# Performance work log

Measured on AMD Instinct MI355X. Metric: run time of the kernel, lower is better.

## Reference

```python
import jax, jax.numpy as jnp
import numpy as np

N = 100000
NFEAT = 512
NHID = 256
NCLASS = 40
E = 1600000
K = 10          # nlayers propagation hops
ALPHA = 0.1


def setup_inputs() -> dict:
    key = jax.random.key(0)
    ks = jax.random.split(key, 8)
    x = jax.random.normal(ks[0], (N, NFEAT), dtype=jnp.float32)
    edge_src = jax.random.randint(ks[1], (E,), 0, N, dtype=jnp.int32)
    edge_dst = jax.random.randint(ks[2], (E,), 0, N, dtype=jnp.int32)
    # roughly row-stochastic-scale edge values (avg degree ~16)
    edge_val = jax.random.uniform(ks[3], (E,), dtype=jnp.float32) * (1.0 / 16.0)
    stdv1 = 1.0 / np.sqrt(NFEAT)
    W1 = jax.random.uniform(ks[4], (NFEAT, NHID), minval=-stdv1, maxval=stdv1, dtype=jnp.float32)
    b1 = jax.random.uniform(ks[5], (NHID,), minval=-stdv1, maxval=stdv1, dtype=jnp.float32)
    stdv2 = 1.0 / np.sqrt(NHID)
    W2 = jax.random.uniform(ks[6], (NHID, NCLASS), minval=-stdv2, maxval=stdv2, dtype=jnp.float32)
    b2 = jax.random.uniform(ks[7], (NCLASS,), minval=-stdv2, maxval=stdv2, dtype=jnp.float32)
    return {"x": x, "edge_src": edge_src, "edge_dst": edge_dst, "edge_val": edge_val,
            "W1": W1, "b1": b1, "W2": W2, "b2": b2}


def _spmm(edge_src, edge_dst, edge_val, z):
    # sparse adj @ z via gather + segment-sum scatter: out[dst] += val * z[src]
    msgs = edge_val[:, None] * z[edge_src]          # [E, C]
    return jax.ops.segment_sum(msgs, edge_dst, num_segments=N)


def reference(x, edge_src, edge_dst, edge_val, W1, b1, W2, b2):
    # MLP transform (dropout is identity in eval mode)
    h = jax.nn.relu(x @ W1 + b1)                    # [N, NHID]
    h = h @ W2 + b2                                 # [N, NCLASS]
    # APPNP propagation: z <- (1-alpha) * A z + alpha * h
    def step(z, _):
        z = _spmm(edge_src, edge_dst, edge_val, z) * (1.0 - ALPHA) + ALPHA * h
        return z, None
    z, _ = jax.lax.scan(step, h, None, length=K)
    return jax.nn.log_softmax(z, axis=1)
```

## Files before the change

kernel.cpp:

```cpp
#include <hip/hip_runtime.h>
#include <hip/hip_bf16.h>
#include <math.h>

#define NN     100000
#define NFEATD 512
#define NHIDD  256
#define NCLS   40
#define NE     1600000
#define KHOP   10

typedef __attribute__((ext_vector_type(8))) short short8;
typedef __attribute__((ext_vector_type(4))) float floatx4;

static __device__ __forceinline__ float bf2f(unsigned int u) {
  unsigned int x = u << 16;
  float f;
  __builtin_memcpy(&f, &x, 4);
  return f;
}
static __device__ __forceinline__ unsigned short f2bf(float f) {
  unsigned int x;
  __builtin_memcpy(&x, &f, 4);
  x = (x + 0x7fffu + ((x >> 16) & 1u)) >> 16;
  return (unsigned short)x;
}
static __device__ __forceinline__ void bf8_to_f(const uint4 u, float* f) {
  unsigned int a0 = u.x, a1 = u.y, a2 = u.z, a3 = u.w;
  unsigned int t;
  t = a0 << 16;          __builtin_memcpy(&f[0], &t, 4);
  t = a0 & 0xffff0000u;  __builtin_memcpy(&f[1], &t, 4);
  t = a1 << 16;          __builtin_memcpy(&f[2], &t, 4);
  t = a1 & 0xffff0000u;  __builtin_memcpy(&f[3], &t, 4);
  t = a2 << 16;          __builtin_memcpy(&f[4], &t, 4);
  t = a2 & 0xffff0000u;  __builtin_memcpy(&f[5], &t, 4);
  t = a3 << 16;          __builtin_memcpy(&f[6], &t, 4);
  t = a3 & 0xffff0000u;  __builtin_memcpy(&f[7], &t, 4);
}

__global__ __launch_bounds__(256) void wt_kernel(const float* __restrict__ W1,
                                                 unsigned short* __restrict__ Wt) {
  int i = blockIdx.x * 256 + threadIdx.x;
  int k = i >> 8;
  int n = i & 255;
  Wt[n * 512 + k] = f2bf(W1[i]);
}

__global__ __launch_bounds__(256) void gemm1_stream_kernel(
    const float* __restrict__ x, const unsigned short* __restrict__ Wt,
    const float* __restrict__ b1, unsigned short* __restrict__ h1) {
  __shared__ __align__(16) unsigned short hs[128 * 128];
  const int tid = threadIdx.x;
  const int lane = tid & 63;
  const int w = tid >> 6;
  const int m = lane & 15;
  const int q = lane >> 4;

  int b = blockIdx.x;
  int g = b >> 4, slot = b & 15;
  int xcol = slot >> 3;
  int y = g * 8 + (slot & 7);
  if (y >= 782) return;
  const int r0 = y * 128 + w * 32;
  const int c0 = xcol * 128;

  const float* arow[2];
#pragma unroll
  for (int i = 0; i < 2; ++i) {
    int gr = r0 + i * 16 + m;
    arow[i] = x + (size_t)(gr < NN ? gr : 0) * NFEATD + q * 8;
  }
  const unsigned short* brow = Wt + (c0 + m) * NFEATD + q * 8;

  floatx4 acc[2][8];
#pragma unroll
  for (int i = 0; i < 2; ++i)
#pragma unroll
    for (int j = 0; j < 8; ++j) acc[i][j] = (floatx4){0.f, 0.f, 0.f, 0.f};

  float4 apf[2][2][2];
#pragma unroll
  for (int par = 0; par < 2; ++par)
#pragma unroll
    for (int i = 0; i < 2; ++i) {
      apf[par][i][0] = *(const float4*)(arow[i] + par * 32);
      apf[par][i][1] = *(const float4*)(arow[i] + par * 32 + 4);
    }

#pragma unroll
  for (int s = 0; s < 16; ++s) {
    const int par = s & 1;
    short8 bfr[8];
#pragma unroll
    for (int j = 0; j < 8; ++j)
      bfr[j] = *(const short8*)(brow + j * 16 * NFEATD + s * 32);
    short8 af[2];
#pragma unroll
    for (int i = 0; i < 2; ++i) {
      float4 lo = apf[par][i][0], hi = apf[par][i][1];
      short8 t;
      t[0] = (short)f2bf(lo.x);
      t[1] = (short)f2bf(lo.y);
      t[2] = (short)f2bf(lo.z);
      t[3] = (short)f2bf(lo.w);
      t[4] = (short)f2bf(hi.x);
      t[5] = (short)f2bf(hi.y);
      t[6] = (short)f2bf(hi.z);
      t[7] = (short)f2bf(hi.w);
      af[i] = t;
    }
    if (s + 2 < 16) {
#pragma unroll
      for (int i = 0; i < 2; ++i) {
        apf[par][i][0] = *(const float4*)(arow[i] + (s + 2) * 32);
        apf[par][i][1] = *(const float4*)(arow[i] + (s + 2) * 32 + 4);
      }
    }
#pragma unroll
    for (int i = 0; i < 2; ++i)
#pragma unroll
      for (int j = 0; j < 8; ++j)
        acc[i][j] =
            __builtin_amdgcn_mfma_f32_16x16x32_bf16(af[i], bfr[j], acc[i][j], 0, 0, 0);
  }

  float bias[8];
#pragma unroll
  for (int j = 0; j < 8; ++j) bias[j] = b1[c0 + j * 16 + m];
#pragma unroll
  for (int i = 0; i < 2; ++i)
#pragma unroll
    for (int r = 0; r < 4; ++r) {
      int rl = w * 32 + i * 16 + q * 4 + r;
#pragma unroll
      for (int j = 0; j < 8; ++j) {
        float v = acc[i][j][r] + bias[j];
        hs[rl * 128 + j * 16 + m] = f2bf(fmaxf(v, 0.f));
      }
    }
  __syncthreads();
#pragma unroll
  for (int rep = 0; rep < 8; ++rep) {
    int idx = rep * 256 + tid;
    int row = idx >> 4;
    int grow = y * 128 + row;
    uint4 v = *(const uint4*)&hs[idx * 8];
    if (grow < NN)
      *(uint4*)(h1 + grow * NHIDD + c0 + (idx & 15) * 8) = v;
  }
}

__global__ __launch_bounds__(256) void gemm2_kernel(
    const unsigned short* __restrict__ h1, const float* __restrict__ W2,
    const float* __restrict__ b2, unsigned short* __restrict__ hb) {
  __shared__ float w2s[NHIDD * NCLS];
  __shared__ float b2s[NCLS];
  __shared__ unsigned short h1s[64 * 264];
  const int tid = threadIdx.x;
  const int r0 = blockIdx.x * 64;
  for (int i = tid; i < NHIDD * NCLS; i += 256) w2s[i] = W2[i];
  if (tid < NCLS) b2s[tid] = b2[tid];
#pragma unroll
  for (int q = 0; q < 8; ++q) {
    int l = tid + q * 256;
    int lr = l >> 5;
    int lc = (l & 31) << 3;
    int row = r0 + lr;
    uint4 v = make_uint4(0, 0, 0, 0);
    if (row < NN) v = *(const uint4*)(h1 + row * NHIDD + lc);
    *(uint4*)&h1s[lr * 264 + lc] = v;
  }
  __syncthreads();
  const int lr = tid >> 2;
  const int cq = (tid & 3) * 10;
  float acc[10];
#pragma unroll
  for (int j = 0; j < 10; ++j) acc[j] = 0.f;
#pragma unroll 4
  for (int k = 0; k < NHIDD; k += 2) {
    unsigned int hp = *(const unsigned int*)&h1s[lr * 264 + k];
    float a0 = bf2f(hp & 0xffffu);
    float a1 = bf2f(hp >> 16);
    const float* w0 = &w2s[k * NCLS + cq];
    const float* w1 = &w2s[(k + 1) * NCLS + cq];
#pragma unroll
    for (int j = 0; j < 10; ++j)
      acc[j] = fmaf(a1, w1[j], fmaf(a0, w0[j], acc[j]));
  }
  int row = r0 + lr;
  if (row < NN) {
#pragma unroll
    for (int jj = 0; jj < 5; ++jj) {
      unsigned int u = (unsigned int)f2bf(acc[2 * jj] + b2s[cq + 2 * jj]) |
                       ((unsigned int)f2bf(acc[2 * jj + 1] + b2s[cq + 2 * jj + 1]) << 16);
      *(unsigned int*)&hb[row * NCLS + cq + 2 * jj] = u;
    }
  }
}

__global__ __launch_bounds__(256) void zero_kernel(int* __restrict__ p, int n) {
  int i = blockIdx.x * 256 + threadIdx.x;
  if (i < n) p[i] = 0;
}
__global__ __launch_bounds__(256) void count_kernel(const int* __restrict__ edst,
                                                    int* __restrict__ counts) {
  int e = blockIdx.x * 256 + threadIdx.x;
  if (e < NE) atomicAdd(&counts[edst[e]], 1);
}
__global__ __launch_bounds__(256) void hist_kernel(const int* __restrict__ counts,
                                                   int* __restrict__ binoff) {
  __shared__ int lhist[64];
  int tid = threadIdx.x;
  if (tid < 64) lhist[tid] = 0;
  __syncthreads();
  int r = blockIdx.x * 256 + tid;
  if (r < NN) {
    int d = counts[r];
    if (d > 63) d = 63;
    atomicAdd(&lhist[d], 1);
  }
  __syncthreads();
  if (tid < 64) {
    int c = lhist[tid];
    if (c) atomicAdd(&binoff[tid], c);
  }
}
__global__ __launch_bounds__(64) void binscan_kernel(int* __restrict__ binoff) {
  __shared__ int s[64];
  int t = threadIdx.x;
  s[t] = binoff[t];
  __syncthreads();
  if (t == 0) {
    int run = 0;
    for (int i = 0; i < 64; ++i) {
      int c = s[i];
      s[i] = run;
      run += c;
    }
  }
  __syncthreads();
  binoff[t] = s[t];
}
__global__ __launch_bounds__(256) void scatter_rows_kernel(
    const int* __restrict__ counts, int* __restrict__ binoff,
    int* __restrict__ perm, int* __restrict__ spos) {
  __shared__ int lhist[64];
  __shared__ int lbase[64];
  int tid = threadIdx.x;
  if (tid < 64) lhist[tid] = 0;
  __syncthreads();
  int r = blockIdx.x * 256 + tid;
  int d = 0, lrank = 0;
  bool valid = (r < NN);
  if (valid) {
    d = counts[r];
    if (d > 63) d = 63;
    lrank = atomicAdd(&lhist[d], 1);
  }
  __syncthreads();
  if (tid < 64) {
    int c = lhist[tid];
    lbase[tid] = c ? atomicAdd(&binoff[tid], c) : 0;
  }
  __syncthreads();
  if (valid) {
    int pos = lbase[d] + lrank;
    perm[pos] = r;
    spos[r] = pos;
  }
}
__global__ __launch_bounds__(256) void scan_blocks_kernel(
    const int* __restrict__ counts, const int* __restrict__ perm,
    int* __restrict__ srs, int* __restrict__ bsum) {
  __shared__ int s[256];
  int gid = blockIdx.x * 256 + threadIdx.x;
  int v = (gid < NN) ? counts[perm[gid]] : 0;
  s[threadIdx.x] = v;
  __syncthreads();
  for (int off = 1; off < 256; off <<= 1) {
    int t = (threadIdx.x >= off) ? s[threadIdx.x - off] : 0;
    __syncthreads();
    s[threadIdx.x] += t;
    __syncthreads();
  }
  if (gid < NN) srs[gid + 1] = s[threadIdx.x];
  if (threadIdx.x == 255) bsum[blockIdx.x] = s[255];
}
#define NB 391
__global__ __launch_bounds__(512) void scan_sums_kernel(int* __restrict__ bsum) {
  __shared__ int s[512];
  int tid = threadIdx.x;
  int v = (tid < NB) ? bsum[tid] : 0;
  s[tid] = v;
  __syncthreads();
  for (int off = 1; off < 512; off <<= 1) {
    int t = (tid >= off) ? s[tid - off] : 0;
    __syncthreads();
    s[tid] += t;
    __syncthreads();
  }
  if (tid < NB) bsum[tid] = (tid == 0) ? 0 : s[tid - 1];
}
__global__ __launch_bounds__(256) void add_off_kernel(int* __restrict__ srs,
                                                      const int* __restrict__ bsum) {
  int gid = blockIdx.x * 256 + threadIdx.x;
  if (gid < NN) srs[gid + 1] += bsum[blockIdx.x];
  if (gid == 0) srs[0] = 0;
}
__global__ __launch_bounds__(256) void scatter_kernel(
    const int* __restrict__ esrc, const int* __restrict__ edst,
    const float* __restrict__ eval, const int* __restrict__ srs,
    const int* __restrict__ spos, int* __restrict__ cursor,
    int2* __restrict__ csr_pair) {
  int e = blockIdx.x * 256 + threadIdx.x;
  if (e < NE) {
    int p = spos[edst[e]];
    int idx = srs[p] + atomicAdd(&cursor[p], 1);
    csr_pair[idx] = make_int2(esrc[e], __float_as_int(eval[e]));
  }
}

__global__ __launch_bounds__(256) void prop_kernel(
    const int* __restrict__ srs, const int* __restrict__ perm,
    const int2* __restrict__ csr_pair, const unsigned short* __restrict__ zi,
    const unsigned short* __restrict__ hb, unsigned short* __restrict__ zo) {
  int t = blockIdx.x * 256 + threadIdx.x;
  if (t >= NN * 5) return;
  unsigned int p = (unsigned int)t / 5u;
  int cg8 = (t - (int)p * 5) * 8;
  int e0 = srs[p], e1 = srs[p + 1];
  int r = perm[p];
  float acc[8];
#pragma unroll
  for (int j = 0; j < 8; ++j) acc[j] = 0.f;

  int e = e0;
  for (; e + 8 <= e1; e += 8) {
    int2 pr[8];
#pragma unroll
    for (int q = 0; q < 8; ++q) pr[q] = csr_pair[e + q];
    uint4 g[8];
#pragma unroll
    for (int q = 0; q < 8; ++q)
      g[q] = *(const uint4*)(zi + pr[q].x * NCLS + cg8);
#pragma unroll
    for (int q = 0; q < 8; ++q) {
      float zf[8];
      bf8_to_f(g[q], zf);
      float v = __int_as_float(pr[q].y);
#pragma unroll
      for (int j = 0; j < 8; ++j) acc[j] = fmaf(v, zf[j], acc[j]);
    }
  }
  for (; e < e1; ++e) {
    int2 pr = csr_pair[e];
    uint4 g = *(const uint4*)(zi + pr.x * NCLS + cg8);
    float zf[8];
    bf8_to_f(g, zf);
    float v = __int_as_float(pr.y);
#pragma unroll
    for (int j = 0; j < 8; ++j) acc[j] = fmaf(v, zf[j], acc[j]);
  }

  uint4 hu = *(const uint4*)(hb + r * NCLS + cg8);
  float hf[8];
  bf8_to_f(hu, hf);
  uint4 o;
  unsigned int wv[4];
#pragma unroll
  for (int i = 0; i < 4; ++i) {
    unsigned int lo = f2bf(0.9f * acc[2 * i] + 0.1f * hf[2 * i]);
    unsigned int hi = f2bf(0.9f * acc[2 * i + 1] + 0.1f * hf[2 * i + 1]);
    wv[i] = lo | (hi << 16);
  }
  o.x = wv[0];
  o.y = wv[1];
  o.z = wv[2];
  o.w = wv[3];
  *(uint4*)(zo + r * NCLS + cg8) = o;
}

__global__ __launch_bounds__(256) void lsm_kernel(const unsigned short* __restrict__ zf,
                                                  float* __restrict__ out) {
  int r = blockIdx.x * 256 + threadIdx.x;
  if (r >= NN) return;
  float v[NCLS];
#pragma unroll
  for (int q = 0; q < 5; ++q) {
    uint4 u = *(const uint4*)(zf + r * NCLS + q * 8);
    bf8_to_f(u, v + q * 8);
  }
  float m = v[0];
#pragma unroll
  for (int i = 1; i < NCLS; ++i) m = fmaxf(m, v[i]);
  float ssum = 0.f;
#pragma unroll
  for (int i = 0; i < NCLS; ++i) ssum += expf(v[i] - m);
  float lse = m + logf(ssum);
#pragma unroll
  for (int q = 0; q < 10; ++q) {
    float4 o;
    o.x = v[q * 4 + 0] - lse;
    o.y = v[q * 4 + 1] - lse;
    o.z = v[q * 4 + 2] - lse;
    o.w = v[q * 4 + 3] - lse;
    *(float4*)(out + r * NCLS + q * 4) = o;
  }
}

extern "C" void kernel_launch(void* const* d_in, const int* in_sizes, int n_in,
                              void* d_out, int out_size, void* d_ws, size_t ws_size,
                              hipStream_t stream) {
  const float* x = (const float*)d_in[0];
  const int* esrc = (const int*)d_in[1];
  const int* edst = (const int*)d_in[2];
  const float* eval = (const float*)d_in[3];
  const float* W1 = (const float*)d_in[4];
  const float* b1 = (const float*)d_in[5];
  const float* W2 = (const float*)d_in[6];
  const float* b2 = (const float*)d_in[7];
  float* out = (float*)d_out;
  char* ws = (char*)d_ws;

  unsigned short* hb = (unsigned short*)(ws + 0);
  unsigned short* zB0 = (unsigned short*)(ws + 8000000);
  unsigned short* zB1 = (unsigned short*)(ws + 16000000);
  unsigned short* Wt = (unsigned short*)(ws + 24000000);
  unsigned short* h1 = (unsigned short*)(ws + 24400000);
  int* counts = (int*)(ws + 75600000);
  int* cursor = (int*)(ws + 76000000);
  int* srs = (int*)(ws + 76400000);
  int* bsum = (int*)(ws + 76800064);
  int* binoff = (int*)(ws + 76802112);
  int* perm = (int*)(ws + 76802624);
  int* spos = (int*)(ws + 77202624);
  int2* csr_pair = (int2*)(ws + 77602624);

  zero_kernel<<<(2 * NN + 255) / 256, 256, 0, stream>>>(counts, 2 * NN);
  zero_kernel<<<1, 256, 0, stream>>>(binoff, 64);

  wt_kernel<<<(NFEATD * NHIDD) / 256, 256, 0, stream>>>(W1, Wt);
  gemm1_stream_kernel<<<1568, 256, 0, stream>>>(x, Wt, b1, h1);
  gemm2_kernel<<<(NN + 63) / 64, 256, 0, stream>>>(h1, W2, b2, hb);

  count_kernel<<<(NE + 255) / 256, 256, 0, stream>>>(edst, counts);
  hist_kernel<<<(NN + 255) / 256, 256, 0, stream>>>(counts, binoff);
  binscan_kernel<<<1, 64, 0, stream>>>(binoff);
  scatter_rows_kernel<<<(NN + 255) / 256, 256, 0, stream>>>(counts, binoff, perm, spos);
  scan_blocks_kernel<<<NB, 256, 0, stream>>>(counts, perm, srs, bsum);
  scan_sums_kernel<<<1, 512, 0, stream>>>(bsum);
  add_off_kernel<<<NB, 256, 0, stream>>>(srs, bsum);
  scatter_kernel<<<(NE + 255) / 256, 256, 0, stream>>>(esrc, edst, eval, srs, spos,
                                                       cursor, csr_pair);

  const unsigned short* zin = hb;
  unsigned short* zout = zB0;
  for (int i = 0; i < KHOP; ++i) {
    prop_kernel<<<(NN * 5 + 255) / 256, 256, 0, stream>>>(srs, perm, csr_pair,
                                                          zin, hb, zout);
    if (i == 0) {
      zin = zB0;
      zout = zB1;
    } else {
      unsigned short* t = (unsigned short*)zin;
      zin = zout;
      zout = t;
    }
  }

  lsm_kernel<<<(NN + 255) / 256, 256, 0, stream>>>(zB1, out);
}
```

Measured before the change: 1.072 ms.

## Fuse both MLP GEMMs into one kernel, keeping hidden activations in registers

Merges the first GEMM (x@W1+b1, relu) and the second GEMM (@W2+b2) into one kernel over 64-row tiles. The hidden activations stay in MFMA accumulators instead of being written to and re-read from a 51MB bf16 buffer. W1 is re-laid out in k-chunks of 8 and staged through double-buffered LDS tiles. The second GEMM becomes per-lane FMAs followed by cross-quad shuffle reductions. In exchange, each block keeps the full 256-wide hidden row, which raises register pressure and lowers occupancy, and the W2 stage runs on scalar FMAs.

```diff
diff --git a/kernel.cpp b/kernel.cpp
--- a/kernel.cpp
+++ b/kernel.cpp
@@ -38,161 +38,159 @@
 }
 
 __global__ __launch_bounds__(256) void wt_kernel(const float* __restrict__ W1,
-                                                 unsigned short* __restrict__ Wt) {
+                                                 unsigned short* __restrict__ Wt2) {
   int i = blockIdx.x * 256 + threadIdx.x;
   int k = i >> 8;
   int n = i & 255;
-  Wt[n * 512 + k] = f2bf(W1[i]);
-}
-
-__global__ __launch_bounds__(256) void gemm1_stream_kernel(
-    const float* __restrict__ x, const unsigned short* __restrict__ Wt,
-    const float* __restrict__ b1, unsigned short* __restrict__ h1) {
-  __shared__ __align__(16) unsigned short hs[128 * 128];
+  Wt2[(k >> 3) * 2048 + n * 8 + (k & 7)] = f2bf(W1[i]);
+}
+
+__global__ __launch_bounds__(256) void mlp_fused_kernel(
+    const float* __restrict__ x, const unsigned short* __restrict__ Wt2,
+    const float* __restrict__ b1, const float* __restrict__ W2,
+    const float* __restrict__ b2, unsigned short* __restrict__ hb) {
+  __shared__ __align__(16) char smem[45056];
+  __shared__ float b1s[256];
+  __shared__ float b2s[64];
   const int tid = threadIdx.x;
   const int lane = tid & 63;
   const int w = tid >> 6;
   const int m = lane & 15;
-  const int q = lane >> 4;
-
-  int b = blockIdx.x;
-  int g = b >> 4, slot = b & 15;
-  int xcol = slot >> 3;
-  int y = g * 8 + (slot & 7);
-  if (y >= 782) return;
-  const int r0 = y * 128 + w * 32;
-  const int c0 = xcol * 128;
-
-  const float* arow[2];
-#pragma unroll
-  for (int i = 0; i < 2; ++i) {
-    int gr = r0 + i * 16 + m;
-    arow[i] = x + (size_t)(gr < NN ? gr : 0) * NFEATD + q * 8;
-  }
-  const unsigned short* brow = Wt + (c0 + m) * NFEATD + q * 8;
-
-  floatx4 acc[2][8];
-#pragma unroll
-  for (int i = 0; i < 2; ++i)
-#pragma unroll
-    for (int j = 0; j < 8; ++j) acc[i][j] = (floatx4){0.f, 0.f, 0.f, 0.f};
-
-  float4 apf[2][2][2];
-#pragma unroll
-  for (int par = 0; par < 2; ++par)
-#pragma unroll
-    for (int i = 0; i < 2; ++i) {
-      apf[par][i][0] = *(const float4*)(arow[i] + par * 32);
-      apf[par][i][1] = *(const float4*)(arow[i] + par * 32 + 4);
-    }
-
-#pragma unroll
-  for (int s = 0; s < 16; ++s) {
-    const int par = s & 1;
-    short8 bfr[8];
-#pragma unroll
-    for (int j = 0; j < 8; ++j)
-      bfr[j] = *(const short8*)(brow + j * 16 * NFEATD + s * 32);
-    short8 af[2];
-#pragma unroll
-    for (int i = 0; i < 2; ++i) {
-      float4 lo = apf[par][i][0], hi = apf[par][i][1];
-      short8 t;
-      t[0] = (short)f2bf(lo.x);
-      t[1] = (short)f2bf(lo.y);
-      t[2] = (short)f2bf(lo.z);
-      t[3] = (short)f2bf(lo.w);
-      t[4] = (short)f2bf(hi.x);
-      t[5] = (short)f2bf(hi.y);
-      t[6] = (short)f2bf(hi.z);
-      t[7] = (short)f2bf(hi.w);
-      af[i] = t;
-    }
-    if (s + 2 < 16) {
-#pragma unroll
-      for (int i = 0; i < 2; ++i) {
-        apf[par][i][0] = *(const float4*)(arow[i] + (s + 2) * 32);
-        apf[par][i][1] = *(const float4*)(arow[i] + (s + 2) * 32 + 4);
+  const int quad = lane >> 4;
+  const int r0 = blockIdx.x * 64;
+
+  b1s[tid] = b1[tid];
+
+  const int sx_row = tid >> 2;
+  const int sx_q = tid & 3;
+  int gxrow = r0 + sx_row;
+  if (gxrow >= NN) gxrow = NN - 1;
+  const float* xsrc = x + (size_t)gxrow * NFEATD + sx_q * 8;
+  const int sx_chunk = sx_q * 64 + sx_row;
+  const unsigned short* wsrc = Wt2 + tid * 8;
+
+  unsigned short* xs0 = (unsigned short*)(smem);
+  unsigned short* wts0 = (unsigned short*)(smem + 4096);
+  unsigned short* xs1 = (unsigned short*)(smem + 20480);
+  unsigned short* wts1 = (unsigned short*)(smem + 20480 + 4096);
+
+  floatx4 acc[16];
+#pragma unroll
+  for (int i = 0; i < 16; ++i) acc[i] = (floatx4){0.f, 0.f, 0.f, 0.f};
+
+  float4 xr[2][2];
+  uint4 wr_[2][4];
+#pragma unroll
+  for (int t = 0; t < 2; ++t) {
+    const int kt = t * 32;
+    xr[t][0] = *(const float4*)(xsrc + kt);
+    xr[t][1] = *(const float4*)(xsrc + kt + 4);
+#pragma unroll
+    for (int c = 0; c < 4; ++c)
+      wr_[t][c] = *(const uint4*)(wsrc + ((kt >> 3) + c) * 2048);
+  }
+
+#pragma unroll
+  for (int t = 0; t < 16; ++t) {
+    const int p = t & 1;
+    unsigned short* xsp = p ? xs1 : xs0;
+    unsigned short* wtsp = p ? wts1 : wts0;
+    {
+      short8 xo;
+      xo[0] = (short)f2bf(xr[p][0].x);
+      xo[1] = (short)f2bf(xr[p][0].y);
+      xo[2] = (short)f2bf(xr[p][0].z);
+      xo[3] = (short)f2bf(xr[p][0].w);
+      xo[4] = (short)f2bf(xr[p][1].x);
+      xo[5] = (short)f2bf(xr[p][1].y);
+      xo[6] = (short)f2bf(xr[p][1].z);
+      xo[7] = (short)f2bf(xr[p][1].w);
+      *(short8*)(xsp + sx_chunk * 8) = xo;
+#pragma unroll
+      for (int c = 0; c < 4; ++c)
+        *(uint4*)(wtsp + (c * 256 + tid) * 8) = wr_[p][c];
+    }
+    if (t + 2 < 16) {
+      const int kt = (t + 2) * 32;
+      xr[p][0] = *(const float4*)(xsrc + kt);
+      xr[p][1] = *(const float4*)(xsrc + kt + 4);
+#pragma unroll
+      for (int c = 0; c < 4; ++c)
+        wr_[p][c] = *(const uint4*)(wsrc + ((kt >> 3) + c) * 2048);
+    }
+    __syncthreads();
+    short8 xf = *(const short8*)(xsp + (quad * 64 + w * 16 + m) * 8);
+#pragma unroll
+    for (int i = 0; i < 16; ++i) {
+      short8 af = *(const short8*)(wtsp + (quad * 256 + i * 16 + m) * 8);
+      acc[i] = __builtin_amdgcn_mfma_f32_16x16x32_bf16(af, xf, acc[i], 0, 0, 0);
+    }
+  }
+
+  __syncthreads();
+  {
+    float* W2s = (float*)smem;
+    const float* wrow = W2 + tid * 40;
+    float4 tmp[10];
+#pragma unroll
+    for (int i2 = 0; i2 < 10; ++i2) tmp[i2] = *(const float4*)(wrow + i2 * 4);
+#pragma unroll
+    for (int i2 = 0; i2 < 10; ++i2) *(float4*)&W2s[tid * 44 + i2 * 4] = tmp[i2];
+    if (tid < NCLS) b2s[tid] = b2[tid];
+  }
+  __syncthreads();
+
+#pragma unroll
+  for (int i = 0; i < 16; ++i)
+#pragma unroll
+    for (int r = 0; r < 4; ++r)
+      acc[i][r] = fmaxf(acc[i][r] + b1s[i * 16 + quad * 4 + r], 0.f);
+
+  const float* W2s = (const float*)smem;
+  const int grow = r0 + w * 16 + m;
+  for (int c = 0; c < 5; ++c) {
+    const int c0 = c * 8;
+    float pa[8];
+#pragma unroll
+    for (int j = 0; j < 8; ++j) pa[j] = 0.f;
+#pragma unroll
+    for (int i = 0; i < 16; ++i) {
+#pragma unroll
+      for (int r = 0; r < 4; ++r) {
+        const int hid = i * 16 + quad * 4 + r;
+        const float hv = acc[i][r];
+        const float* wv = W2s + hid * 44 + c0;
+        float4 wa = *(const float4*)wv;
+        float4 wb = *(const float4*)(wv + 4);
+        pa[0] = fmaf(hv, wa.x, pa[0]);
+        pa[1] = fmaf(hv, wa.y, pa[1]);
+        pa[2] = fmaf(hv, wa.z, pa[2]);
+        pa[3] = fmaf(hv, wa.w, pa[3]);
+        pa[4] = fmaf(hv, wb.x, pa[4]);
+        pa[5] = fmaf(hv, wb.y, pa[5]);
+        pa[6] = fmaf(hv, wb.z, pa[6]);
+        pa[7] = fmaf(hv, wb.w, pa[7]);
       }
     }
 #pragma unroll
-    for (int i = 0; i < 2; ++i)
-#pragma unroll
-      for (int j = 0; j < 8; ++j)
-        acc[i][j] =
-            __builtin_amdgcn_mfma_f32_16x16x32_bf16(af[i], bfr[j], acc[i][j], 0, 0, 0);
-  }
-
-  float bias[8];
-#pragma unroll
-  for (int j = 0; j < 8; ++j) bias[j] = b1[c0 + j * 16 + m];
-#pragma unroll
-  for (int i = 0; i < 2; ++i)
-#pragma unroll
-    for (int r = 0; r < 4; ++r) {
-      int rl = w * 32 + i * 16 + q * 4 + r;
-#pragma unroll
-      for (int j = 0; j < 8; ++j) {
-        float v = acc[i][j][r] + bias[j];
-        hs[rl * 128 + j * 16 + m] = f2bf(fmaxf(v, 0.f));
+    for (int j = 0; j < 8; ++j) {
+      pa[j] += __shfl_xor(pa[j], 16);
+      pa[j] += __shfl_xor(pa[j], 32);
+    }
+    if (quad == 0 && grow < NN) {
+      unsigned int u[4];
+#pragma unroll
+      for (int jj = 0; jj < 4; ++jj) {
+        unsigned int lo = f2bf(pa[2 * jj] + b2s[c0 + 2 * jj]);
+        unsigned int hi = f2bf(pa[2 * jj + 1] + b2s[c0 + 2 * jj + 1]);
+        u[jj] = lo | (hi << 16);
       }
-    }
-  __syncthreads();
-#pragma unroll
-  for (int rep = 0; rep < 8; ++rep) {
-    int idx = rep * 256 + tid;
-    int row = idx >> 4;
-    int grow = y * 128 + row;
-    uint4 v = *(const uint4*)&hs[idx * 8];
-    if (grow < NN)
-      *(uint4*)(h1 + grow * NHIDD + c0 + (idx & 15) * 8) = v;
-  }
-}
-
-__global__ __launch_bounds__(256) void gemm2_kernel(
-    const unsigned short* __restrict__ h1, const float* __restrict__ W2,
-    const float* __restrict__ b2, unsigned short* __restrict__ hb) {
-  __shared__ float w2s[NHIDD * NCLS];
-  __shared__ float b2s[NCLS];
-  __shared__ unsigned short h1s[64 * 264];
-  const int tid = threadIdx.x;
-  const int r0 = blockIdx.x * 64;
-  for (int i = tid; i < NHIDD * NCLS; i += 256) w2s[i] = W2[i];
-  if (tid < NCLS) b2s[tid] = b2[tid];
-#pragma unroll
-  for (int q = 0; q < 8; ++q) {
-    int l = tid + q * 256;
-    int lr = l >> 5;
-    int lc = (l & 31) << 3;
-    int row = r0 + lr;
-    uint4 v = make_uint4(0, 0, 0, 0);
-    if (row < NN) v = *(const uint4*)(h1 + row * NHIDD + lc);
-    *(uint4*)&h1s[lr * 264 + lc] = v;
-  }
-  __syncthreads();
-  const int lr = tid >> 2;
-  const int cq = (tid & 3) * 10;
-  float acc[10];
-#pragma unroll
-  for (int j = 0; j < 10; ++j) acc[j] = 0.f;
-#pragma unroll 4
-  for (int k = 0; k < NHIDD; k += 2) {
-    unsigned int hp = *(const unsigned int*)&h1s[lr * 264 + k];
-    float a0 = bf2f(hp & 0xffffu);
-    float a1 = bf2f(hp >> 16);
-    const float* w0 = &w2s[k * NCLS + cq];
-    const float* w1 = &w2s[(k + 1) * NCLS + cq];
-#pragma unroll
-    for (int j = 0; j < 10; ++j)
-      acc[j] = fmaf(a1, w1[j], fmaf(a0, w0[j], acc[j]));
-  }
-  int row = r0 + lr;
-  if (row < NN) {
-#pragma unroll
-    for (int jj = 0; jj < 5; ++jj) {
-      unsigned int u = (unsigned int)f2bf(acc[2 * jj] + b2s[cq + 2 * jj]) |
-                       ((unsigned int)f2bf(acc[2 * jj + 1] + b2s[cq + 2 * jj + 1]) << 16);
-      *(unsigned int*)&hb[row * NCLS + cq + 2 * jj] = u;
+      uint4 o;
+      o.x = u[0];
+      o.y = u[1];
+      o.z = u[2];
+      o.w = u[3];
+      *(uint4*)(hb + (size_t)grow * NCLS + c0) = o;
     }
   }
 }
@@ -424,8 +422,7 @@
   unsigned short* hb = (unsigned short*)(ws + 0);
   unsigned short* zB0 = (unsigned short*)(ws + 8000000);
   unsigned short* zB1 = (unsigned short*)(ws + 16000000);
-  unsigned short* Wt = (unsigned short*)(ws + 24000000);
-  unsigned short* h1 = (unsigned short*)(ws + 24400000);
+  unsigned short* Wt2 = (unsigned short*)(ws + 24000000);
   int* counts = (int*)(ws + 75600000);
   int* cursor = (int*)(ws + 76000000);
   int* srs = (int*)(ws + 76400000);
@@ -438,9 +435,8 @@
   zero_kernel<<<(2 * NN + 255) / 256, 256, 0, stream>>>(counts, 2 * NN);
   zero_kernel<<<1, 256, 0, stream>>>(binoff, 64);
 
-  wt_kernel<<<(NFEATD * NHIDD) / 256, 256, 0, stream>>>(W1, Wt);
-  gemm1_stream_kernel<<<1568, 256, 0, stream>>>(x, Wt, b1, h1);
-  gemm2_kernel<<<(NN + 63) / 64, 256, 0, stream>>>(h1, W2, b2, hb);
+  wt_kernel<<<(NFEATD * NHIDD) / 256, 256, 0, stream>>>(W1, Wt2);
+  mlp_fused_kernel<<<(NN + 63) / 64, 256, 0, stream>>>(x, Wt2, b1, W2, b2, hb);
 
   count_kernel<<<(NE + 255) / 256, 256, 0, stream>>>(edst, counts);
   hist_kernel<<<(NN + 255) / 256, 256, 0, stream>>>(counts, binoff);
```

New measurement: 1.107 ms. +3.2%, slower.
